# Performance work log

Hardware: AMD Instinct MI355X
Metric: run time of the kernel (lower is better)

## Reference

```python
import jax, jax.numpy as jnp
import numpy as np

N_VERTS = 100000
N_FACES = 200000
C = 512


def setup_inputs() -> dict:
    key = jax.random.key(0)
    ks = jax.random.split(key, 12)
    x = jax.random.normal(ks[0], (1, N_VERTS, C), dtype=jnp.float32) * 0.1
    verts = jax.random.normal(ks[1], (N_VERTS, 3), dtype=jnp.float32)
    faces = jax.random.randint(ks[2], (N_FACES, 3), 0, N_VERTS, dtype=jnp.int32)
    def lin(k, fan_in, fan_out):
        return jax.random.normal(k, (fan_in, fan_out), dtype=jnp.float32) / np.sqrt(fan_in)
    return {
        "x": x, "verts": verts, "faces": faces,
        "W1": lin(ks[3], C, C),    "b1": jnp.zeros((C,), jnp.float32),
        "W2": lin(ks[4], C, 512),  "b2": jnp.zeros((512,), jnp.float32),
        "W3": lin(ks[5], 512, 256),"b3": jnp.zeros((256,), jnp.float32),
        "W4": lin(ks[6], 256, 12), "b4": jnp.zeros((12,), jnp.float32),
    }


def special_procrustes(M):
    # roma.special_procrustes: nearest rotation in SO(3) to M, batched [F,3,3]
    U, S, Vh = jnp.linalg.svd(M)
    det = jnp.linalg.det(jnp.matmul(U, Vh))  # [F]
    D = jnp.stack([jnp.ones_like(det), jnp.ones_like(det), det], axis=-1)  # [F,3]
    return jnp.matmul(U * D[:, None, :], Vh)


def reference(x, verts, faces, W1, b1, W2, b2, W3, b3, W4, b4):
    N = verts.shape[0]
    F = faces.shape[0]
    # prism base: gather 3 vertex positions per face -> [F,3,3]
    prism_base = verts[faces]
    # gather features of the 3 face vertices and mean over them -> [F,C]
    feat = x[0][faces].mean(axis=1)
    # mlp_refine
    h = jax.nn.relu(feat @ W1 + b1)
    h = jax.nn.relu(h @ W2 + b2)
    h = jax.nn.relu(h @ W3 + b3)
    out = h @ W4 + b4  # [F,12]
    # batched 3x3 Procrustes rotation + translation
    rotations = special_procrustes(out[:, :9].reshape(F, 3, 3))
    translations = out[:, 9:]  # [F,3]
    transformed_prism = jnp.matmul(prism_base, rotations) + translations[:, None, :]  # [F,3,3]
    # scatter-add back to vertices with per-vertex face-count normalization
    flat_idx = faces.reshape(-1)  # [3F]
    summed = jax.ops.segment_sum(transformed_prism.reshape(-1, 3), flat_idx, num_segments=N)
    counts = jax.ops.segment_sum(jnp.ones((3 * F,), jnp.float32), flat_idx, num_segments=N)
    features = summed / jnp.clip(counts, 1.0)[:, None]  # [N,3]
    return features[None], transformed_prism, rotations
```

## Files before the change

### kernel.cpp

```cpp
#include <hip/hip_runtime.h>
#include <hip/hip_bf16.h>
#include <stdint.h>

typedef __attribute__((ext_vector_type(8))) short short8;
typedef __attribute__((ext_vector_type(4))) float f32x4;
typedef __attribute__((ext_vector_type(4))) unsigned short u16x4;

__device__ __forceinline__ unsigned short f2bf(float x) {
    union { float f; uint32_t u; } v; v.f = x;
    uint32_t u = v.u;
    uint32_t r = (u + 0x7FFFu + ((u >> 16) & 1u)) >> 16;
    return (unsigned short)r;
}
__device__ __forceinline__ float bf2f(unsigned short h) {
    union { uint32_t u; float f; } v; v.u = ((uint32_t)h) << 16;
    return v.f;
}
__device__ __forceinline__ void split_rne(float f, unsigned short& hi, unsigned short& lo) {
    __hip_bfloat16 h = __float2bfloat16(f);
    union { __hip_bfloat16 b; unsigned short u; } ch; ch.b = h; hi = ch.u;
    float hf = __bfloat162float(h);
    __hip_bfloat16 l = __float2bfloat16(f - hf);
    union { __hip_bfloat16 b; unsigned short u; } cl; cl.b = l; lo = cl.u;
}

__device__ __forceinline__ void gld_lds16(const void* g, void* s) {
    __builtin_amdgcn_global_load_lds(
        (const __attribute__((address_space(1))) void*)(uintptr_t)g,
        (__attribute__((address_space(3))) void*)(uint32_t)(uintptr_t)s,
        16, 0, 0);
}

__device__ __forceinline__ f32x4 mfma16(short8 a, short8 b, f32x4 c) {
    return __builtin_amdgcn_mfma_f32_16x16x32_bf16(a, b, c, 0, 0, 0);
}

__global__ void prep_weights(const float* __restrict__ W1, const float* __restrict__ W2,
                             const float* __restrict__ W3,
                             unsigned short* __restrict__ w1h, unsigned short* __restrict__ w1l,
                             unsigned short* __restrict__ w2h, unsigned short* __restrict__ w2l,
                             unsigned short* __restrict__ w3h, unsigned short* __restrict__ w3l,
                             float* __restrict__ sums, float* __restrict__ counts, int nverts) {
    int t = blockIdx.x * 256 + threadIdx.x;
    if (t < nverts * 3) sums[t] = 0.0f;
    if (t < nverts)     counts[t] = 0.0f;
    float v; unsigned short *ph, *pl; size_t o;
    if (t < 262144) {
        int k = t >> 9, n = t & 511;
        v = W1[t]; o = (size_t)n * 512 + k; ph = w1h; pl = w1l;
    } else if (t < 524288) {
        int u = t - 262144; int k = u >> 9, n = u & 511;
        v = W2[u]; o = (size_t)n * 512 + k; ph = w2h; pl = w2l;
    } else if (t < 655360) {
        int u = t - 524288; int k = u >> 8, n = u & 255;
        v = W3[u]; o = (size_t)n * 512 + k; ph = w3h; pl = w3l;
    } else return;
    unsigned short hi, lo;
    split_rne(v, hi, lo);
    ph[o] = hi; pl[o] = lo;
}

__global__ void gather_mean(const float* __restrict__ x, const int* __restrict__ faces,
                            unsigned short* __restrict__ Fhi, unsigned short* __restrict__ Flo,
                            int fbase, int fcount, int mrows) {
    int t = blockIdx.x * 256 + threadIdx.x;
    if (t >= (mrows << 7)) return;
    int r = t >> 7;
    int c = (t & 127) << 2;
    f32x4 m = {0.f, 0.f, 0.f, 0.f};
    if (r < fcount) {
        int f = fbase + r;
        int i0 = faces[3 * f], i1 = faces[3 * f + 1], i2 = faces[3 * f + 2];
        f32x4 a = *(const f32x4*)(x + (size_t)i0 * 512 + c);
        f32x4 b = *(const f32x4*)(x + (size_t)i1 * 512 + c);
        f32x4 d = *(const f32x4*)(x + (size_t)i2 * 512 + c);
        m = (a + b + d) * (1.0f / 3.0f);
    }
    u16x4 hv, lv;
#pragma unroll
    for (int j = 0; j < 4; ++j) {
        unsigned short hi, lo;
        split_rne(m[j], hi, lo);
        hv[j] = hi; lv[j] = lo;
    }
    *(u16x4*)(Fhi + (size_t)r * 512 + c) = hv;
    *(u16x4*)(Flo + (size_t)r * 512 + c) = lv;
}

template<int OUT>
__global__ __launch_bounds__(256, 2)
void gemm_pipe(const unsigned short* __restrict__ Ahi, const unsigned short* __restrict__ Alo,
               const unsigned short* __restrict__ Bhi, const unsigned short* __restrict__ Blo,
               const float* __restrict__ bias,
               void* __restrict__ Out0, unsigned short* __restrict__ Olo,
               int N, int K, int nt) {
    __shared__ __align__(16) unsigned short sm[2][4][128 * 32];

    const int tid  = threadIdx.x;
    const int lane = tid & 63;
    const int w    = tid >> 6;
    const int wr = w >> 1, wc = w & 1;

    const int nwg  = gridDim.x;
    const int orig = blockIdx.x;
    const int q = nwg >> 3, r8 = nwg & 7;
    const int xcd = orig & 7, idx = orig >> 3;
    const int wg = (xcd < r8 ? xcd * (q + 1) : r8 * (q + 1) + (xcd - r8) * q) + idx;
    const int m0 = (wg / nt) << 7;
    const int n0 = (wg % nt) << 7;

    f32x4 acc[4][4] = {};

    const int s_lo  = w * 64 + lane;
    const int row0  = s_lo >> 2;
    const int c0    = ((s_lo & 3) - ((row0 >> 1) & 3)) & 3;
    const int s_hi  = 256 + s_lo;
    const int row1  = (s_hi >> 2) & 127;
    const int c1    = ((s_hi & 3) - ((row1 >> 1) & 3)) & 3;

    const uint32_t oA0 = (uint32_t)(m0 + row0) * (uint32_t)K + (c0 << 3);
    const uint32_t oA1 = (uint32_t)(m0 + row1) * (uint32_t)K + (c1 << 3);
    const uint32_t oB0 = (uint32_t)(n0 + row0) * (uint32_t)K + (c0 << 3);
    const uint32_t oB1 = (uint32_t)(n0 + row1) * (uint32_t)K + (c1 << 3);

    auto stage = [&](int b, int t) {
        const uint32_t k0 = t << 5;
        gld_lds16(Ahi + oA0 + k0, &sm[b][0][(w * 64) * 8]);
        gld_lds16(Ahi + oA1 + k0, &sm[b][0][(256 + w * 64) * 8]);
        gld_lds16(Alo + oA0 + k0, &sm[b][1][(w * 64) * 8]);
        gld_lds16(Alo + oA1 + k0, &sm[b][1][(256 + w * 64) * 8]);
        gld_lds16(Bhi + oB0 + k0, &sm[b][2][(w * 64) * 8]);
        gld_lds16(Bhi + oB1 + k0, &sm[b][2][(256 + w * 64) * 8]);
        gld_lds16(Blo + oB0 + k0, &sm[b][3][(w * 64) * 8]);
        gld_lds16(Blo + oB1 + k0, &sm[b][3][(256 + w * 64) * 8]);
    };

    const int NT = K >> 5;
    stage(0, 0);
    stage(1, 1);

    const int kc  = lane >> 4;
    const int rbA = (wr << 6) + (lane & 15);
    const int rbB = (wc << 6) + (lane & 15);

    for (int t = 0; t < NT; ++t) {
        const int cur = t & 1;

        if (t + 1 < NT) asm volatile("s_waitcnt vmcnt(8)" ::: "memory");
        else            asm volatile("s_waitcnt vmcnt(0)" ::: "memory");
        __builtin_amdgcn_s_barrier();

        short8 ah[4], al[4], bh[4], bl[4];
#pragma unroll
        for (int m = 0; m < 4; ++m) {
            const int r   = rbA + (m << 4);
            const int off = r * 32 + (((kc + (r >> 1)) & 3) << 3);
            ah[m] = *(const short8*)&sm[cur][0][off];
            al[m] = *(const short8*)&sm[cur][1][off];
        }
#pragma unroll
        for (int n = 0; n < 4; ++n) {
            const int r   = rbB + (n << 4);
            const int off = r * 32 + (((kc + (r >> 1)) & 3) << 3);
            bh[n] = *(const short8*)&sm[cur][2][off];
            bl[n] = *(const short8*)&sm[cur][3][off];
        }
        asm volatile("s_waitcnt lgkmcnt(0)" ::: "memory");
        __builtin_amdgcn_sched_barrier(0);
        __builtin_amdgcn_s_barrier();

        if (t + 2 < NT) stage(cur, t + 2);

        __builtin_amdgcn_s_setprio(1);
#pragma unroll
        for (int m = 0; m < 4; ++m)
#pragma unroll
            for (int n = 0; n < 4; ++n)
                acc[m][n] = mfma16(ah[m], bh[n], acc[m][n]);
#pragma unroll
        for (int m = 0; m < 4; ++m)
#pragma unroll
            for (int n = 0; n < 4; ++n)
                acc[m][n] = mfma16(al[m], bh[n], acc[m][n]);
#pragma unroll
        for (int m = 0; m < 4; ++m)
#pragma unroll
            for (int n = 0; n < 4; ++n)
                acc[m][n] = mfma16(ah[m], bl[n], acc[m][n]);
        __builtin_amdgcn_s_setprio(0);
    }

#pragma unroll
    for (int n = 0; n < 4; ++n) {
        const int col = n0 + (wc << 6) + (n << 4) + (lane & 15);
        const float bv = (OUT == 1) ? 0.0f : bias[col];
#pragma unroll
        for (int m = 0; m < 4; ++m) {
            const int rbase = m0 + (wr << 6) + (m << 4) + ((lane >> 4) << 2);
#pragma unroll
            for (int j = 0; j < 4; ++j) {
                const size_t o = (size_t)(rbase + j) * N + col;
                if (OUT == 1) {
                    ((float*)Out0)[o] = acc[m][n][j];
                } else if (OUT == 2) {
                    ((float*)Out0)[o] = fmaxf(acc[m][n][j] + bv, 0.0f);
                } else {
                    float v = fmaxf(acc[m][n][j] + bv, 0.0f);
                    unsigned short hi, lo;
                    split_rne(v, hi, lo);
                    ((unsigned short*)Out0)[o] = hi;
                    Olo[o] = lo;
                }
            }
        }
    }
}

__global__ __launch_bounds__(256, 2)
void gemm_l1(const float* __restrict__ X,
             const unsigned short* __restrict__ Bhi, const unsigned short* __restrict__ Blo,
             float* __restrict__ Out,
             int N, int K, int nt, int nvalid) {
    __shared__ __align__(16) unsigned short sm[2][4][128 * 32];

    const int tid  = threadIdx.x;
    const int lane = tid & 63;
    const int w    = tid >> 6;
    const int wr = w >> 1, wc = w & 1;

    const int nwg  = gridDim.x;
    const int orig = blockIdx.x;
    const int q = nwg >> 3, r8 = nwg & 7;
    const int xcd = orig & 7, idx = orig >> 3;
    const int wg = (xcd < r8 ? xcd * (q + 1) : r8 * (q + 1) + (xcd - r8) * q) + idx;
    const int m0 = (wg / nt) << 7;
    const int n0 = (wg % nt) << 7;

    f32x4 acc[4][4] = {};

    int adst[2], avalid[2];
    uint32_t xoff[2];
#pragma unroll
    for (int i = 0; i < 2; ++i) {
        const int s   = i * 256 + tid;
        const int row = s >> 2;
        const int c   = s & 3;
        adst[i]   = row * 32 + (((c + (row >> 1)) & 3) << 3);
        avalid[i] = (m0 + row) < nvalid;
        xoff[i]   = (uint32_t)(avalid[i] ? (m0 + row) : 0) * (uint32_t)K + (c << 3);
    }
    const int s_lo  = w * 64 + lane;
    const int row0  = s_lo >> 2;
    const int c0    = ((s_lo & 3) - ((row0 >> 1) & 3)) & 3;
    const int s_hi  = 256 + s_lo;
    const int row1  = (s_hi >> 2) & 127;
    const int c1    = ((s_hi & 3) - ((row1 >> 1) & 3)) & 3;
    const uint32_t oB0 = (uint32_t)(n0 + row0) * (uint32_t)K + (c0 << 3);
    const uint32_t oB1 = (uint32_t)(n0 + row1) * (uint32_t)K + (c1 << 3);

    f32x4 fA[2][2];

    auto issueA = [&](int t) {
        const uint32_t k0 = t << 5;
#pragma unroll
        for (int i = 0; i < 2; ++i) {
            const float* src = X + xoff[i] + k0;
            fA[i][0] = *(const f32x4*)src;
            fA[i][1] = *(const f32x4*)(src + 4);
        }
    };
    auto issueB = [&](int b, int t) {
        const uint32_t k0 = t << 5;
        gld_lds16(Bhi + oB0 + k0, &sm[b][2][(w * 64) * 8]);
        gld_lds16(Bhi + oB1 + k0, &sm[b][2][(256 + w * 64) * 8]);
        gld_lds16(Blo + oB0 + k0, &sm[b][3][(w * 64) * 8]);
        gld_lds16(Blo + oB1 + k0, &sm[b][3][(256 + w * 64) * 8]);
    };
    auto cvtWriteA = [&](int b) {
#pragma unroll
        for (int i = 0; i < 2; ++i) {
            short8 hv, lv;
#pragma unroll
            for (int j = 0; j < 8; ++j) {
                float f = avalid[i] ? fA[i][j >> 2][j & 3] : 0.0f;
                unsigned short hi, lo;
                split_rne(f, hi, lo);
                hv[j] = (short)hi;
                lv[j] = (short)lo;
            }
            *(short8*)&sm[b][0][adst[i]] = hv;
            *(short8*)&sm[b][1][adst[i]] = lv;
        }
    };

    const int NT = K >> 5;
    issueA(0); issueB(0, 0);
    asm volatile("s_waitcnt vmcnt(4)" ::: "memory");
    cvtWriteA(0);
    issueA(1); issueB(1, 1);
    asm volatile("s_waitcnt vmcnt(4)" ::: "memory");
    cvtWriteA(1);
    asm volatile("s_waitcnt lgkmcnt(0)" ::: "memory");

    const int kc  = lane >> 4;
    const int rbA = (wr << 6) + (lane & 15);
    const int rbB = (wc << 6) + (lane & 15);

    for (int t = 0; t < NT; ++t) {
        const int cur = t & 1;

        if (t + 1 < NT) asm volatile("s_waitcnt vmcnt(4)" ::: "memory");
        else            asm volatile("s_waitcnt vmcnt(0)" ::: "memory");
        __builtin_amdgcn_s_barrier();

        if (t + 2 < NT) issueA(t + 2);

        short8 ah[4], al[4], bh[4], bl[4];
#pragma unroll
        for (int m = 0; m < 4; ++m) {
            const int r   = rbA + (m << 4);
            const int off = r * 32 + (((kc + (r >> 1)) & 3) << 3);
            ah[m] = *(const short8*)&sm[cur][0][off];
            al[m] = *(const short8*)&sm[cur][1][off];
        }
#pragma unroll
        for (int n = 0; n < 4; ++n) {
            const int r   = rbB + (n << 4);
            const int off = r * 32 + (((kc + (r >> 1)) & 3) << 3);
            bh[n] = *(const short8*)&sm[cur][2][off];
            bl[n] = *(const short8*)&sm[cur][3][off];
        }
        asm volatile("s_waitcnt lgkmcnt(0)" ::: "memory");
        __builtin_amdgcn_sched_barrier(0);
        __builtin_amdgcn_s_barrier();

        if (t + 2 < NT) issueB(cur, t + 2);

        __builtin_amdgcn_s_setprio(1);
#pragma unroll
        for (int m = 0; m < 4; ++m)
#pragma unroll
            for (int n = 0; n < 4; ++n)
                acc[m][n] = mfma16(ah[m], bh[n], acc[m][n]);
#pragma unroll
        for (int m = 0; m < 4; ++m)
#pragma unroll
            for (int n = 0; n < 4; ++n)
                acc[m][n] = mfma16(al[m], bh[n], acc[m][n]);
#pragma unroll
        for (int m = 0; m < 4; ++m)
#pragma unroll
            for (int n = 0; n < 4; ++n)
                acc[m][n] = mfma16(ah[m], bl[n], acc[m][n]);
        __builtin_amdgcn_s_setprio(0);

        if (t + 2 < NT) {
            asm volatile("s_waitcnt vmcnt(4)" ::: "memory");
            cvtWriteA(cur);
        }
    }

#pragma unroll
    for (int n = 0; n < 4; ++n) {
        const int col = n0 + (wc << 6) + (n << 4) + (lane & 15);
#pragma unroll
        for (int m = 0; m < 4; ++m) {
            const int rbase = m0 + (wr << 6) + (m << 4) + ((lane >> 4) << 2);
#pragma unroll
            for (int j = 0; j < 4; ++j)
                Out[(size_t)(rbase + j) * N + col] = acc[m][n][j];
        }
    }
}

__global__ __launch_bounds__(256, 2)
void gemm_l2g(const float* __restrict__ Y, const int* __restrict__ faces,
              const float* __restrict__ b1,
              const unsigned short* __restrict__ Bhi, const unsigned short* __restrict__ Blo,
              const float* __restrict__ bias2,
              unsigned short* __restrict__ Ohi, unsigned short* __restrict__ Olo,
              int N, int K, int nt, int nvalid) {
    __shared__ __align__(16) unsigned short sm[2][4][128 * 32];

    const int tid  = threadIdx.x;
    const int lane = tid & 63;
    const int w    = tid >> 6;
    const int wr = w >> 1, wc = w & 1;

    const int nwg  = gridDim.x;
    const int orig = blockIdx.x;
    const int q = nwg >> 3, r8 = nwg & 7;
    const int xcd = orig & 7, idx = orig >> 3;
    const int wg = (xcd < r8 ? xcd * (q + 1) : r8 * (q + 1) + (xcd - r8) * q) + idx;
    const int m0 = (wg / nt) << 7;
    const int n0 = (wg % nt) << 7;

    f32x4 acc[4][4] = {};

    int adst[2], avalid[2];
    uint32_t yoff[2][3];
    const int achk = tid & 3;
#pragma unroll
    for (int i = 0; i < 2; ++i) {
        const int s   = i * 256 + tid;
        const int row = s >> 2;
        adst[i]   = row * 32 + (((achk + (row >> 1)) & 3) << 3);
        const int gf  = m0 + row;
        avalid[i] = gf < nvalid;
        const int gfs = avalid[i] ? gf : 0;
#pragma unroll
        for (int r = 0; r < 3; ++r)
            yoff[i][r] = (uint32_t)faces[3 * gfs + r] * (uint32_t)K;
    }
    const int s_lo  = w * 64 + lane;
    const int row0  = s_lo >> 2;
    const int c0    = ((s_lo & 3) - ((row0 >> 1) & 3)) & 3;
    const int s_hi  = 256 + s_lo;
    const int row1  = (s_hi >> 2) & 127;
    const int c1    = ((s_hi & 3) - ((row1 >> 1) & 3)) & 3;
    const uint32_t oB0 = (uint32_t)(n0 + row0) * (uint32_t)K + (c0 << 3);
    const uint32_t oB1 = (uint32_t)(n0 + row1) * (uint32_t)K + (c1 << 3);

    f32x4 fA[2][3][2];
    f32x4 fb[2];

    auto issueA = [&](int t) {
        const uint32_t koff = (uint32_t)(t << 5) + (achk << 3);
#pragma unroll
        for (int i = 0; i < 2; ++i) {
#pragma unroll
            for (int r = 0; r < 3; ++r) {
                const float* src = Y + yoff[i][r] + koff;
                fA[i][r][0] = *(const f32x4*)src;
                fA[i][r][1] = *(const f32x4*)(src + 4);
            }
        }
        fb[0] = *(const f32x4*)(b1 + koff);
        fb[1] = *(const f32x4*)(b1 + koff + 4);
    };
    auto issueB = [&](int b, int t) {
        const uint32_t k0 = t << 5;
        gld_lds16(Bhi + oB0 + k0, &sm[b][2][(w * 64) * 8]);
        gld_lds16(Bhi + oB1 + k0, &sm[b][2][(256 + w * 64) * 8]);
        gld_lds16(Blo + oB0 + k0, &sm[b][3][(w * 64) * 8]);
        gld_lds16(Blo + oB1 + k0, &sm[b][3][(256 + w * 64) * 8]);
    };
    auto cvtWriteA = [&](int b) {
        const float third = 1.0f / 3.0f;
#pragma unroll
        for (int i = 0; i < 2; ++i) {
            short8 hv, lv;
#pragma unroll
            for (int j = 0; j < 8; ++j) {
                const int h = j >> 2, e = j & 3;
                float f = 0.0f;
                if (avalid[i]) {
                    f = fmaf(fA[i][0][h][e] + fA[i][1][h][e] + fA[i][2][h][e], third, fb[h][e]);
                    f = fmaxf(f, 0.0f);
                }
                unsigned short hi, lo;
                split_rne(f, hi, lo);
                hv[j] = (short)hi;
                lv[j] = (short)lo;
            }
            *(short8*)&sm[b][0][adst[i]] = hv;
            *(short8*)&sm[b][1][adst[i]] = lv;
        }
    };

    const int NT = K >> 5;
    issueA(0); issueB(0, 0);
    asm volatile("s_waitcnt vmcnt(4)" ::: "memory");
    cvtWriteA(0);
    issueA(1); issueB(1, 1);
    asm volatile("s_waitcnt vmcnt(4)" ::: "memory");
    cvtWriteA(1);
    asm volatile("s_waitcnt lgkmcnt(0)" ::: "memory");

    const int kc  = lane >> 4;
    const int rbA = (wr << 6) + (lane & 15);
    const int rbB = (wc << 6) + (lane & 15);

    for (int t = 0; t < NT; ++t) {
        const int cur = t & 1;

        if (t + 1 < NT) asm volatile("s_waitcnt vmcnt(4)" ::: "memory");
        else            asm volatile("s_waitcnt vmcnt(0)" ::: "memory");
        __builtin_amdgcn_s_barrier();

        if (t + 2 < NT) issueA(t + 2);

        short8 ah[4], al[4], bh[4], bl[4];
#pragma unroll
        for (int m = 0; m < 4; ++m) {
            const int r   = rbA + (m << 4);
            const int off = r * 32 + (((kc + (r >> 1)) & 3) << 3);
            ah[m] = *(const short8*)&sm[cur][0][off];
            al[m] = *(const short8*)&sm[cur][1][off];
        }
#pragma unroll
        for (int n = 0; n < 4; ++n) {
            const int r   = rbB + (n << 4);
            const int off = r * 32 + (((kc + (r >> 1)) & 3) << 3);
            bh[n] = *(const short8*)&sm[cur][2][off];
            bl[n] = *(const short8*)&sm[cur][3][off];
        }
        asm volatile("s_waitcnt lgkmcnt(0)" ::: "memory");
        __builtin_amdgcn_sched_barrier(0);
        __builtin_amdgcn_s_barrier();

        if (t + 2 < NT) issueB(cur, t + 2);

        __builtin_amdgcn_s_setprio(1);
#pragma unroll
        for (int m = 0; m < 4; ++m)
#pragma unroll
            for (int n = 0; n < 4; ++n)
                acc[m][n] = mfma16(ah[m], bh[n], acc[m][n]);
#pragma unroll
        for (int m = 0; m < 4; ++m)
#pragma unroll
            for (int n = 0; n < 4; ++n)
                acc[m][n] = mfma16(al[m], bh[n], acc[m][n]);
#pragma unroll
        for (int m = 0; m < 4; ++m)
#pragma unroll
            for (int n = 0; n < 4; ++n)
                acc[m][n] = mfma16(ah[m], bl[n], acc[m][n]);
        __builtin_amdgcn_s_setprio(0);

        if (t + 2 < NT) {
            asm volatile("s_waitcnt vmcnt(4)" ::: "memory");
            cvtWriteA(cur);
        }
    }

#pragma unroll
    for (int n = 0; n < 4; ++n) {
        const int col = n0 + (wc << 6) + (n << 4) + (lane & 15);
        const float bv = bias2[col];
#pragma unroll
        for (int m = 0; m < 4; ++m) {
            const int rbase = m0 + (wr << 6) + (m << 4) + ((lane >> 4) << 2);
#pragma unroll
            for (int j = 0; j < 4; ++j) {
                const size_t o = (size_t)(rbase + j) * N + col;
                float v = fmaxf(acc[m][n][j] + bv, 0.0f);
                unsigned short hi, lo;
                split_rne(v, hi, lo);
                Ohi[o] = hi;
                Olo[o] = lo;
            }
        }
    }
}

#define JROT(app, aqq, apq, apz, aqz, vp0, vp1, vp2, vq0, vq1, vq2) do {          \
    float _apq = (apq);                                                            \
    if (fabsf(_apq) > 1e-30f) {                                                    \
        float _tau = ((aqq) - (app)) / (2.0f * _apq);                              \
        float _t = copysignf(1.0f, _tau) / (fabsf(_tau) + sqrtf(1.0f + _tau*_tau));\
        float _c = 1.0f / sqrtf(1.0f + _t*_t);                                     \
        float _s = _t * _c;                                                        \
        (app) = (app) - _t * _apq;                                                 \
        (aqq) = (aqq) + _t * _apq;                                                 \
        (apq) = 0.0f;                                                              \
        float _pz = (apz), _qz = (aqz);                                            \
        (apz) = _c * _pz - _s * _qz;                                               \
        (aqz) = _s * _pz + _c * _qz;                                               \
        float _x;                                                                  \
        _x = (vp0); (vp0) = _c*_x - _s*(vq0); (vq0) = _s*_x + _c*(vq0);            \
        _x = (vp1); (vp1) = _c*_x - _s*(vq1); (vq1) = _s*_x + _c*(vq1);            \
        _x = (vp2); (vp2) = _c*_x - _s*(vq2); (vq2) = _s*_x + _c*(vq2);            \
    }                                                                              \
} while (0)

#define SWAP3(la, lb, x0, y0, z0, x1, y1, z1) do {                \
    float _tm;                                                    \
    _tm = la; la = lb; lb = _tm;                                  \
    _tm = x0; x0 = x1; x1 = _tm;                                  \
    _tm = y0; y0 = y1; y1 = _tm;                                  \
    _tm = z0; z0 = z1; z1 = _tm;                                  \
} while (0)

__global__ void face_kernel(const float* __restrict__ H3,
                            const float* __restrict__ W4, const float* __restrict__ b4,
                            const float* __restrict__ verts, const int* __restrict__ faces,
                            float* __restrict__ out_tp, float* __restrict__ out_rot,
                            float* __restrict__ sums, float* __restrict__ counts,
                            int fbase, int fcount) {
    __shared__ float sW[256 * 12 + 12];
    for (int i = threadIdx.x; i < 256 * 12 + 12; i += 256)
        sW[i] = (i < 256 * 12) ? W4[i] : b4[i - 256 * 12];
    __syncthreads();

    const int r = blockIdx.x * 256 + threadIdx.x;
    if (r >= fcount) return;
    const int f = fbase + r;

    float o[12];
#pragma unroll
    for (int n = 0; n < 12; ++n) o[n] = sW[3072 + n];
    const f32x4* ph = (const f32x4*)(H3 + (size_t)r * 256);
    for (int kb = 0; kb < 64; ++kb) {
        f32x4 hv = ph[kb];
#pragma unroll
        for (int kk = 0; kk < 4; ++kk) {
            float val = hv[kk];
            const float* wrow = &sW[(kb * 4 + kk) * 12];
#pragma unroll
            for (int n = 0; n < 12; ++n) o[n] = fmaf(val, wrow[n], o[n]);
        }
    }

    const float M00=o[0], M01=o[1], M02=o[2];
    const float M10=o[3], M11=o[4], M12=o[5];
    const float M20=o[6], M21=o[7], M22=o[8];
    const float t0 =o[9], t1 =o[10], t2 =o[11];

    float a00 = M00*M00 + M10*M10 + M20*M20;
    float a11 = M01*M01 + M11*M11 + M21*M21;
    float a22 = M02*M02 + M12*M12 + M22*M22;
    float a01 = M00*M01 + M10*M11 + M20*M21;
    float a02 = M00*M02 + M10*M12 + M20*M22;
    float a12 = M01*M02 + M11*M12 + M21*M22;

    float v00=1.f, v01=0.f, v02=0.f;
    float v10=0.f, v11=1.f, v12=0.f;
    float v20=0.f, v21=0.f, v22=1.f;
#pragma unroll
    for (int sweep = 0; sweep < 5; ++sweep) {
        JROT(a00, a11, a01, a02, a12, v00, v10, v20, v01, v11, v21);
        JROT(a00, a22, a02, a01, a12, v00, v10, v20, v02, v12, v22);
        JROT(a11, a22, a12, a01, a02, v01, v11, v21, v02, v12, v22);
    }
    float l0 = a00, l1 = a11, l2 = a22;
    if (l0 < l1) SWAP3(l0, l1, v00, v10, v20, v01, v11, v21);
    if (l0 < l2) SWAP3(l0, l2, v00, v10, v20, v02, v12, v22);
    if (l1 < l2) SWAP3(l1, l2, v01, v11, v21, v02, v12, v22);

    float b1x = M00*v00 + M01*v10 + M02*v20;
    float b1y = M10*v00 + M11*v10 + M12*v20;
    float b1z = M20*v00 + M21*v10 + M22*v20;
    float b2x = M00*v01 + M01*v11 + M02*v21;
    float b2y = M10*v01 + M11*v11 + M12*v21;
    float b2z = M20*v01 + M21*v11 + M22*v21;

    float n1 = sqrtf(b1x*b1x + b1y*b1y + b1z*b1z);
    float u1x, u1y, u1z;
    if (n1 > 1e-25f) { float in = 1.0f / n1; u1x = b1x*in; u1y = b1y*in; u1z = b1z*in; }
    else             { u1x = 1.f; u1y = 0.f; u1z = 0.f; }

    float dp  = b2x*u1x + b2y*u1y + b2z*u1z;
    float w2x = b2x - dp*u1x, w2y = b2y - dp*u1y, w2z = b2z - dp*u1z;
    float n2  = sqrtf(w2x*w2x + w2y*w2y + w2z*w2z);
    float u2x, u2y, u2z;
    if (n2 > 1e-25f) { float in = 1.0f / n2; u2x = w2x*in; u2y = w2y*in; u2z = w2z*in; }
    else {
        float ex = (fabsf(u1x) < 0.9f) ? 1.f : 0.f;
        float ey = 1.f - ex;
        float cx = -u1z * ey, cy = u1z * ex, cz = u1x * ey - u1y * ex;
        float cn = rsqrtf(cx*cx + cy*cy + cz*cz);
        u2x = cx * cn; u2y = cy * cn; u2z = cz * cn;
    }
    float u3x = u1y*u2z - u1z*u2y;
    float u3y = u1z*u2x - u1x*u2z;
    float u3z = u1x*u2y - u1y*u2x;

    float dv = v00*(v11*v22 - v12*v21) - v01*(v10*v22 - v12*v20) + v02*(v10*v21 - v11*v20);
    if (dv < 0.f) { v02 = -v02; v12 = -v12; v22 = -v22; }

    float R00 = u1x*v00 + u2x*v01 + u3x*v02;
    float R01 = u1x*v10 + u2x*v11 + u3x*v12;
    float R02 = u1x*v20 + u2x*v21 + u3x*v22;
    float R10 = u1y*v00 + u2y*v01 + u3y*v02;
    float R11 = u1y*v10 + u2y*v11 + u3y*v12;
    float R12 = u1y*v20 + u2y*v21 + u3y*v22;
    float R20 = u1z*v00 + u2z*v01 + u3z*v02;
    float R21 = u1z*v10 + u2z*v11 + u3z*v12;
    float R22 = u1z*v20 + u2z*v21 + u3z*v22;

    float* rp = out_rot + (size_t)f * 9;
    rp[0]=R00; rp[1]=R01; rp[2]=R02;
    rp[3]=R10; rp[4]=R11; rp[5]=R12;
    rp[6]=R20; rp[7]=R21; rp[8]=R22;

    float* tp = out_tp + (size_t)f * 9;
    const int idx[3] = { faces[3*f], faces[3*f+1], faces[3*f+2] };
#pragma unroll
    for (int j = 0; j < 3; ++j) {
        const int vi = idx[j];
        float px = verts[3*vi], py = verts[3*vi+1], pz = verts[3*vi+2];
        float q0 = px*R00 + py*R10 + pz*R20 + t0;
        float q1 = px*R01 + py*R11 + pz*R21 + t1;
        float q2 = px*R02 + py*R12 + pz*R22 + t2;
        tp[j*3+0] = q0; tp[j*3+1] = q1; tp[j*3+2] = q2;
        atomicAdd(&sums[(size_t)vi*3+0], q0);
        atomicAdd(&sums[(size_t)vi*3+1], q1);
        atomicAdd(&sums[(size_t)vi*3+2], q2);
        atomicAdd(&counts[vi], 1.0f);
    }
}

__global__ void finalize_kernel(float* __restrict__ feats, const float* __restrict__ counts, int nverts) {
    int v = blockIdx.x * 256 + threadIdx.x;
    if (v >= nverts) return;
    float c = fmaxf(counts[v], 1.0f);
    feats[v*3+0] = feats[v*3+0] / c;
    feats[v*3+1] = feats[v*3+1] / c;
    feats[v*3+2] = feats[v*3+2] / c;
}

extern "C" void kernel_launch(void* const* d_in, const int* in_sizes, int n_in,
                              void* d_out, int out_size, void* d_ws, size_t ws_size,
                              hipStream_t stream) {
    const float* x     = (const float*)d_in[0];
    const float* verts = (const float*)d_in[1];
    const int*   faces = (const int*)d_in[2];
    const float* W1 = (const float*)d_in[3];
    const float* b1 = (const float*)d_in[4];
    const float* W2 = (const float*)d_in[5];
    const float* b2 = (const float*)d_in[6];
    const float* W3 = (const float*)d_in[7];
    const float* b3 = (const float*)d_in[8];
    const float* W4 = (const float*)d_in[9];
    const float* b4 = (const float*)d_in[10];

    const int nverts = in_sizes[1] / 3;
    const int nfaces = in_sizes[2] / 3;

    float* out_feats = (float*)d_out;
    float* out_tp    = out_feats + (size_t)nverts * 3;
    float* out_rot   = out_tp + (size_t)nfaces * 9;

    char* ws = (char*)d_ws;
    size_t cur = 0;
    auto carve = [&](size_t bytes) -> void* {
        void* p = ws + cur;
        cur += (bytes + 255) & ~(size_t)255;
        return p;
    };
    unsigned short* w1h = (unsigned short*)carve(512 * 512 * 2);
    unsigned short* w1l = (unsigned short*)carve(512 * 512 * 2);
    unsigned short* w2h = (unsigned short*)carve(512 * 512 * 2);
    unsigned short* w2l = (unsigned short*)carve(512 * 512 * 2);
    unsigned short* w3h = (unsigned short*)carve(256 * 512 * 2);
    unsigned short* w3l = (unsigned short*)carve(256 * 512 * 2);
    float* counts = (float*)carve((size_t)nverts * 4);

    const long MV = ((long)nverts + 127) & ~127L;
    const long MF = ((long)nfaces + 127) & ~127L;
    const size_t szY   = (size_t)MV * 512 * 4;
    const size_t szH2w = (size_t)MF * 512 * 2;
    const size_t szH3f = (size_t)MF * 256 * 4;

    const size_t sR1 = (szY > szH3f) ? szY : szH3f;
    const size_t sR2 = szH2w;
    const size_t sR3 = szH2w;
    const size_t need = cur + sR1 + sR2 + sR3 + 4 * 256;

    prep_weights<<<(655360 + 255) / 256, 256, 0, stream>>>(W1, W2, W3, w1h, w1l, w2h, w2l, w3h, w3l,
                                                           out_feats, counts, nverts);

    if (ws_size >= need) {
        char* R1 = (char*)carve(sR1);
        char* R2 = (char*)carve(sR2);
        char* R3 = (char*)carve(sR3);
        float*          y   = (float*)R1;
        float*          h3  = (float*)R1;
        unsigned short* h2h = (unsigned short*)R2;
        unsigned short* h2l = (unsigned short*)R3;

        gemm_l1<<<(int)(MV / 128) * 4, 256, 0, stream>>>(x, w1h, w1l, y, 512, 512, 4, nverts);

        gemm_l2g<<<(int)(MF / 128) * 4, 256, 0, stream>>>(y, faces, b1, w2h, w2l, b2,
                                                          h2h, h2l, 512, 512, 4, nfaces);

        gemm_pipe<2><<<(int)(MF / 128) * 2, 256, 0, stream>>>(h2h, h2l, w3h, w3l, b3, h3, nullptr, 256, 512, 2);

        face_kernel<<<(nfaces + 255) / 256, 256, 0, stream>>>(h3, W4, b4, verts, faces,
                                                              out_tp, out_rot, out_feats, counts,
                                                              0, nfaces);
    } else {
        long mpad = MF;
        size_t avail = (ws_size > cur) ? (ws_size - cur) : 0;
        long chp = (long)(avail / 4096);
        chp &= ~127L;
        if (chp > mpad) chp = mpad;
        if (chp < 128) chp = 128;
        unsigned short* bAh = (unsigned short*)carve((size_t)chp * 512 * 2);
        unsigned short* bAl = (unsigned short*)carve((size_t)chp * 512 * 2);
        unsigned short* bBh = (unsigned short*)carve((size_t)chp * 512 * 2);
        unsigned short* bBl = (unsigned short*)carve((size_t)chp * 512 * 2);

        for (long base = 0; base < nfaces; base += chp) {
            long rem = (long)nfaces - base;
            int cnt = (int)((rem < chp) ? rem : chp);
            int mc  = (cnt + 127) & ~127;

            gather_mean<<<mc / 2, 256, 0, stream>>>(x, faces, bAh, bAl, (int)base, cnt, mc);
            gemm_pipe<0><<<(mc / 128) * 4, 256, 0, stream>>>(bAh, bAl, w1h, w1l, b1, bBh, bBl, 512, 512, 4);
            gemm_pipe<0><<<(mc / 128) * 4, 256, 0, stream>>>(bBh, bBl, w2h, w2l, b2, bAh, bAl, 512, 512, 4);
            gemm_pipe<2><<<(mc / 128) * 2, 256, 0, stream>>>(bAh, bAl, w3h, w3l, b3, (float*)bBh, nullptr, 256, 512, 2);
            face_kernel<<<(cnt + 255) / 256, 256, 0, stream>>>((float*)bBh, W4, b4, verts, faces,
                                                               out_tp, out_rot, out_feats, counts,
                                                               (int)base, cnt);
        }
    }

    finalize_kernel<<<(nverts + 255) / 256, 256, 0, stream>>>(out_feats, counts, nverts);
}
```

Before: 1.156 ms.

## Restructure gathered layer-2 GEMM to full-width row tiles with direct-global B loads

The gathered second-layer GEMM now processes 64 face rows against all 512 output columns per workgroup, so the vertex-feature gather and mean/bias/ReLU for each face happens once instead of four times across column tiles. B operand fragments are loaded straight from global memory into registers rather than staged through LDS, halving shared memory and dropping B-side waits. The A-side hi/lo bf16 split now uses truncation instead of round-to-nearest, which is cheaper but slightly changes the precision split. The trade-off is heavier global/L2 traffic for the weights and more accumulator registers per wave (4x8 tiles).

```diff
diff --git a/kernel.cpp b/kernel.cpp
--- a/kernel.cpp
+++ b/kernel.cpp
@@ -6,12 +6,6 @@
 typedef __attribute__((ext_vector_type(4))) float f32x4;
 typedef __attribute__((ext_vector_type(4))) unsigned short u16x4;
 
-__device__ __forceinline__ unsigned short f2bf(float x) {
-    union { float f; uint32_t u; } v; v.f = x;
-    uint32_t u = v.u;
-    uint32_t r = (u + 0x7FFFu + ((u >> 16) & 1u)) >> 16;
-    return (unsigned short)r;
-}
 __device__ __forceinline__ float bf2f(unsigned short h) {
     union { uint32_t u; float f; } v; v.u = ((uint32_t)h) << 16;
     return v.f;
@@ -22,6 +16,13 @@
     float hf = __bfloat162float(h);
     __hip_bfloat16 l = __float2bfloat16(f - hf);
     union { __hip_bfloat16 b; unsigned short u; } cl; cl.b = l; lo = cl.u;
+}
+__device__ __forceinline__ void splitT(float f, unsigned short& hi, unsigned short& lo) {
+    union { float f; uint32_t u; } a; a.f = f;
+    hi = (unsigned short)(a.u >> 16);
+    union { uint32_t u; float f; } b; b.u = a.u & 0xFFFF0000u;
+    union { float f; uint32_t u; } c; c.f = f - b.f;
+    lo = (unsigned short)(c.u >> 16);
 }
 
 __device__ __forceinline__ void gld_lds16(const void* g, void* s) {
@@ -284,7 +285,7 @@
             for (int j = 0; j < 8; ++j) {
                 float f = avalid[i] ? fA[i][j >> 2][j & 3] : 0.0f;
                 unsigned short hi, lo;
-                split_rne(f, hi, lo);
+                splitT(f, hi, lo);
                 hv[j] = (short)hi;
                 lv[j] = (short)lo;
             }
@@ -374,143 +375,107 @@
 }
 
 __global__ __launch_bounds__(256, 2)
-void gemm_l2g(const float* __restrict__ Y, const int* __restrict__ faces,
+void gemm_l2w(const float* __restrict__ Y, const int* __restrict__ faces,
               const float* __restrict__ b1,
               const unsigned short* __restrict__ Bhi, const unsigned short* __restrict__ Blo,
               const float* __restrict__ bias2,
               unsigned short* __restrict__ Ohi, unsigned short* __restrict__ Olo,
-              int N, int K, int nt, int nvalid) {
-    __shared__ __align__(16) unsigned short sm[2][4][128 * 32];
+              int K, int nvalid) {
+    __shared__ __align__(16) unsigned short sm[2][2][64 * 32];
 
     const int tid  = threadIdx.x;
     const int lane = tid & 63;
     const int w    = tid >> 6;
-    const int wr = w >> 1, wc = w & 1;
 
     const int nwg  = gridDim.x;
     const int orig = blockIdx.x;
     const int q = nwg >> 3, r8 = nwg & 7;
     const int xcd = orig & 7, idx = orig >> 3;
     const int wg = (xcd < r8 ? xcd * (q + 1) : r8 * (q + 1) + (xcd - r8) * q) + idx;
-    const int m0 = (wg / nt) << 7;
-    const int n0 = (wg % nt) << 7;
-
-    f32x4 acc[4][4] = {};
-
-    int adst[2], avalid[2];
-    uint32_t yoff[2][3];
+    const int m0 = wg << 6;
+
+    f32x4 acc[4][8] = {};
+
+    const int arow = tid >> 2;
     const int achk = tid & 3;
-#pragma unroll
-    for (int i = 0; i < 2; ++i) {
-        const int s   = i * 256 + tid;
-        const int row = s >> 2;
-        adst[i]   = row * 32 + (((achk + (row >> 1)) & 3) << 3);
-        const int gf  = m0 + row;
-        avalid[i] = gf < nvalid;
-        const int gfs = avalid[i] ? gf : 0;
-#pragma unroll
-        for (int r = 0; r < 3; ++r)
-            yoff[i][r] = (uint32_t)faces[3 * gfs + r] * (uint32_t)K;
-    }
-    const int s_lo  = w * 64 + lane;
-    const int row0  = s_lo >> 2;
-    const int c0    = ((s_lo & 3) - ((row0 >> 1) & 3)) & 3;
-    const int s_hi  = 256 + s_lo;
-    const int row1  = (s_hi >> 2) & 127;
-    const int c1    = ((s_hi & 3) - ((row1 >> 1) & 3)) & 3;
-    const uint32_t oB0 = (uint32_t)(n0 + row0) * (uint32_t)K + (c0 << 3);
-    const uint32_t oB1 = (uint32_t)(n0 + row1) * (uint32_t)K + (c1 << 3);
-
-    f32x4 fA[2][3][2];
+    const int adst = arow * 32 + (((achk + (arow >> 1)) & 3) << 3);
+    const int gf   = m0 + arow;
+    const int avalid = gf < nvalid;
+    const int gfs  = avalid ? gf : 0;
+    uint32_t yoff[3];
+#pragma unroll
+    for (int r = 0; r < 3; ++r)
+        yoff[r] = (uint32_t)faces[3 * gfs + r] * (uint32_t)K;
+
+    const uint32_t bBase = (uint32_t)((w << 7) + (lane & 15)) * (uint32_t)K + ((lane >> 4) << 3);
+
+    f32x4 fA[3][2];
     f32x4 fb[2];
 
     auto issueA = [&](int t) {
         const uint32_t koff = (uint32_t)(t << 5) + (achk << 3);
 #pragma unroll
-        for (int i = 0; i < 2; ++i) {
-#pragma unroll
-            for (int r = 0; r < 3; ++r) {
-                const float* src = Y + yoff[i][r] + koff;
-                fA[i][r][0] = *(const f32x4*)src;
-                fA[i][r][1] = *(const f32x4*)(src + 4);
-            }
+        for (int r = 0; r < 3; ++r) {
+            const float* src = Y + yoff[r] + koff;
+            fA[r][0] = *(const f32x4*)src;
+            fA[r][1] = *(const f32x4*)(src + 4);
         }
         fb[0] = *(const f32x4*)(b1 + koff);
         fb[1] = *(const f32x4*)(b1 + koff + 4);
     };
-    auto issueB = [&](int b, int t) {
-        const uint32_t k0 = t << 5;
-        gld_lds16(Bhi + oB0 + k0, &sm[b][2][(w * 64) * 8]);
-        gld_lds16(Bhi + oB1 + k0, &sm[b][2][(256 + w * 64) * 8]);
-        gld_lds16(Blo + oB0 + k0, &sm[b][3][(w * 64) * 8]);
-        gld_lds16(Blo + oB1 + k0, &sm[b][3][(256 + w * 64) * 8]);
+    auto cvtWriteA = [&](int b) {
+        short8 hv, lv;
+#pragma unroll
+        for (int j = 0; j < 8; ++j) {
+            const int h = j >> 2, e = j & 3;
+            float f = 0.0f;
+            if (avalid) {
+                f = fmaf(fA[0][h][e] + fA[1][h][e] + fA[2][h][e], 1.0f / 3.0f, fb[h][e]);
+                f = fmaxf(f, 0.0f);
+            }
+            unsigned short hi, lo;
+            splitT(f, hi, lo);
+            hv[j] = (short)hi;
+            lv[j] = (short)lo;
+        }
+        *(short8*)&sm[b][0][adst] = hv;
+        *(short8*)&sm[b][1][adst] = lv;
     };
-    auto cvtWriteA = [&](int b) {
-        const float third = 1.0f / 3.0f;
-#pragma unroll
-        for (int i = 0; i < 2; ++i) {
-            short8 hv, lv;
-#pragma unroll
-            for (int j = 0; j < 8; ++j) {
-                const int h = j >> 2, e = j & 3;
-                float f = 0.0f;
-                if (avalid[i]) {
-                    f = fmaf(fA[i][0][h][e] + fA[i][1][h][e] + fA[i][2][h][e], third, fb[h][e]);
-                    f = fmaxf(f, 0.0f);
-                }
-                unsigned short hi, lo;
-                split_rne(f, hi, lo);
-                hv[j] = (short)hi;
-                lv[j] = (short)lo;
-            }
-            *(short8*)&sm[b][0][adst[i]] = hv;
-            *(short8*)&sm[b][1][adst[i]] = lv;
-        }
-    };
 
     const int NT = K >> 5;
-    issueA(0); issueB(0, 0);
-    asm volatile("s_waitcnt vmcnt(4)" ::: "memory");
-    cvtWriteA(0);
-    issueA(1); issueB(1, 1);
-    asm volatile("s_waitcnt vmcnt(4)" ::: "memory");
-    cvtWriteA(1);
+    issueA(0); cvtWriteA(0);
+    issueA(1); cvtWriteA(1);
     asm volatile("s_waitcnt lgkmcnt(0)" ::: "memory");
+    __builtin_amdgcn_s_barrier();
 
     const int kc  = lane >> 4;
-    const int rbA = (wr << 6) + (lane & 15);
-    const int rbB = (wc << 6) + (lane & 15);
+    const int rlA = lane & 15;
 
     for (int t = 0; t < NT; ++t) {
         const int cur = t & 1;
-
-        if (t + 1 < NT) asm volatile("s_waitcnt vmcnt(4)" ::: "memory");
-        else            asm volatile("s_waitcnt vmcnt(0)" ::: "memory");
-        __builtin_amdgcn_s_barrier();
+        const uint32_t k0 = (uint32_t)(t << 5);
 
         if (t + 2 < NT) issueA(t + 2);
 
-        short8 ah[4], al[4], bh[4], bl[4];
+        short8 bh[4], bl[4];
+#pragma unroll
+        for (int n = 0; n < 4; ++n) {
+            bh[n] = *(const short8*)(Bhi + bBase + (uint32_t)(n * 16) * (uint32_t)K + k0);
+            bl[n] = *(const short8*)(Blo + bBase + (uint32_t)(n * 16) * (uint32_t)K + k0);
+        }
+
+        short8 ah[4], al[4];
 #pragma unroll
         for (int m = 0; m < 4; ++m) {
-            const int r   = rbA + (m << 4);
+            const int r   = rlA + (m << 4);
             const int off = r * 32 + (((kc + (r >> 1)) & 3) << 3);
             ah[m] = *(const short8*)&sm[cur][0][off];
             al[m] = *(const short8*)&sm[cur][1][off];
         }
-#pragma unroll
-        for (int n = 0; n < 4; ++n) {
-            const int r   = rbB + (n << 4);
-            const int off = r * 32 + (((kc + (r >> 1)) & 3) << 3);
-            bh[n] = *(const short8*)&sm[cur][2][off];
-            bl[n] = *(const short8*)&sm[cur][3][off];
-        }
         asm volatile("s_waitcnt lgkmcnt(0)" ::: "memory");
         __builtin_amdgcn_sched_barrier(0);
         __builtin_amdgcn_s_barrier();
 
-        if (t + 2 < NT) issueB(cur, t + 2);
-
         __builtin_amdgcn_s_setprio(1);
 #pragma unroll
         for (int m = 0; m < 4; ++m)
@@ -529,22 +494,42 @@
                 acc[m][n] = mfma16(ah[m], bl[n], acc[m][n]);
         __builtin_amdgcn_s_setprio(0);
 
-        if (t + 2 < NT) {
-            asm volatile("s_waitcnt vmcnt(4)" ::: "memory");
-            cvtWriteA(cur);
-        }
-    }
-
-#pragma unroll
-    for (int n = 0; n < 4; ++n) {
-        const int col = n0 + (wc << 6) + (n << 4) + (lane & 15);
+#pragma unroll
+        for (int n = 0; n < 4; ++n) {
+            bh[n] = *(const short8*)(Bhi + bBase + (uint32_t)((n + 4) * 16) * (uint32_t)K + k0);
+            bl[n] = *(const short8*)(Blo + bBase + (uint32_t)((n + 4) * 16) * (uint32_t)K + k0);
+        }
+        __builtin_amdgcn_s_setprio(1);
+#pragma unroll
+        for (int m = 0; m < 4; ++m)
+#pragma unroll
+            for (int n = 0; n < 4; ++n)
+                acc[m][4 + n] = mfma16(ah[m], bh[n], acc[m][4 + n]);
+#pragma unroll
+        for (int m = 0; m < 4; ++m)
+#pragma unroll
+            for (int n = 0; n < 4; ++n)
+                acc[m][4 + n] = mfma16(al[m], bh[n], acc[m][4 + n]);
+#pragma unroll
+        for (int m = 0; m < 4; ++m)
+#pragma unroll
+            for (int n = 0; n < 4; ++n)
+                acc[m][4 + n] = mfma16(ah[m], bl[n], acc[m][4 + n]);
+        __builtin_amdgcn_s_setprio(0);
+
+        if (t + 2 < NT) cvtWriteA(cur);
+    }
+
+#pragma unroll
+    for (int n = 0; n < 8; ++n) {
+        const int col = (w << 7) + (n << 4) + (lane & 15);
         const float bv = bias2[col];
 #pragma unroll
         for (int m = 0; m < 4; ++m) {
-            const int rbase = m0 + (wr << 6) + (m << 4) + ((lane >> 4) << 2);
+            const int rbase = m0 + (m << 4) + ((lane >> 4) << 2);
 #pragma unroll
             for (int j = 0; j < 4; ++j) {
-                const size_t o = (size_t)(rbase + j) * N + col;
+                const size_t o = (size_t)(rbase + j) * 512 + col;
                 float v = fmaxf(acc[m][n][j] + bv, 0.0f);
                 unsigned short hi, lo;
                 split_rne(v, hi, lo);
@@ -773,8 +758,8 @@
 
         gemm_l1<<<(int)(MV / 128) * 4, 256, 0, stream>>>(x, w1h, w1l, y, 512, 512, 4, nverts);
 
-        gemm_l2g<<<(int)(MF / 128) * 4, 256, 0, stream>>>(y, faces, b1, w2h, w2l, b2,
-                                                          h2h, h2l, 512, 512, 4, nfaces);
+        gemm_l2w<<<(int)(MF / 64), 256, 0, stream>>>(y, faces, b1, w2h, w2l, b2,
+                                                     h2h, h2l, 512, nfaces);
 
         gemm_pipe<2><<<(int)(MF / 128) * 2, 256, 0, stream>>>(h2h, h2l, w3h, w3l, b3, h3, nullptr, 256, 512, 2);
 
```

Result: slower. 1.182 ms (+2.3%).
